# Optimization experiments

Hardware: AMD Instinct MI355X
Metric: run time of the kernel (lower is better)

The kernel has to match this reference:

```python
import jax, jax.numpy as jnp
import numpy as np

B, C, W = 32, 3, 512
KSIZE = 5
EPS = 8.0
ID_OFFSET = 4.0
SCALE = ID_OFFSET / (W - 1)            # identity_offset / (image_crop - 1)
DEF_OFF = (2.0 + SCALE) / 2.0          # deforming_offset
PIX_W = 2.0 / W                        # pixel width in [-1,1] coords

def _gauss_kernel2d(k):
    sigma = k * 0.15 + 0.35
    half = (k - 1) * 0.5
    x = np.linspace(-half, half, k)
    pdf = np.exp(-0.5 * (x / sigma) ** 2)
    k1 = pdf / pdf.sum()
    return np.outer(k1, k1).astype(np.float32)

def _samp_iden():
    seq = np.arange(-(W - 1), W, 2) / (W - 1.0)   # length W, identity coords
    gx = np.tile(seq, (W, 1))
    gy = gx.T
    return jnp.asarray(np.stack([gx, gy])[None].astype(np.float32))  # [1,2,W,W]

IDEN = _samp_iden()
GKER = jnp.broadcast_to(jnp.asarray(_gauss_kernel2d(KSIZE))[None, None], (2, 1, KSIZE, KSIZE))

def _blur(g):
    p = KSIZE // 2
    g = jnp.pad(g, ((0, 0), (0, 0), (p, p), (p, p)), mode='reflect')
    # depthwise conv over the 2 grid channels (groups=2)
    return jax.lax.conv_general_dilated(g, GKER, (1, 1), 'VALID', feature_group_count=2)

def _forward_grid(prim_grid):
    pg = _blur(prim_grid)
    sg = pg + IDEN                                   # prim -> samp
    # samp -> accu: conv_transpose with [1,-1] == first difference (leading zero)
    s = sg + DEF_OFF
    sx, sy = s[:, :1], s[:, 1:2]
    ax = sx - jnp.concatenate([jnp.zeros_like(sx[..., :1]), sx[..., :-1]], axis=3)
    ay = sy - jnp.concatenate([jnp.zeros_like(sy[:, :, :1]), sy[:, :, :-1]], axis=2)
    ag = jnp.concatenate([ax, ay], axis=1) / SCALE
    ag = jax.nn.relu(ag)                             # accu_clip
    # accu -> samp: conv_transpose with all-ones filter == cumulative sum
    a = ag * SCALE
    sx2 = jnp.cumsum(a[:, :1], axis=3)
    sy2 = jnp.cumsum(a[:, 1:2], axis=2)
    sg = jnp.concatenate([sx2, sy2], axis=1) - DEF_OFF
    pg = jnp.clip(sg - IDEN, -PIX_W * EPS, PIX_W * EPS)  # prim_clip
    return jnp.clip(pg + IDEN, -1.0, 1.0)                # samp_clip (hardtanh)

def _grid_sample(img, grid):
    # img [B,C,W,W], grid [B,W,W,2] in [-1,1]; bilinear, zeros padding, align_corners=True
    x = (grid[..., 0] + 1.0) * 0.5 * (W - 1)
    y = (grid[..., 1] + 1.0) * 0.5 * (W - 1)
    x0 = jnp.floor(x); y0 = jnp.floor(y)
    x1 = x0 + 1.0;     y1 = y0 + 1.0
    wx1 = x - x0; wx0 = 1.0 - wx1
    wy1 = y - y0; wy0 = 1.0 - wy1
    def gather(xi, yi):
        valid = ((xi >= 0) & (xi < W) & (yi >= 0) & (yi < W)).astype(img.dtype)
        xc = jnp.clip(xi, 0, W - 1).astype(jnp.int32)
        yc = jnp.clip(yi, 0, W - 1).astype(jnp.int32)
        v = jax.vmap(lambda im, yy, xx: im[:, yy, xx])(img, yc, xc)  # [B,C,W,W]
        return v * valid[:, None]
    return (gather(x0, y0) * (wx0 * wy0)[:, None] + gather(x1, y0) * (wx1 * wy0)[:, None]
          + gather(x0, y1) * (wx0 * wy1)[:, None] + gather(x1, y1) * (wx1 * wy1)[:, None])

def setup_inputs() -> dict:
    key = jax.random.key(0)
    k1, k2 = jax.random.split(key)
    image = jax.random.normal(k1, (B, C, W, W), dtype=jnp.float32)
    prim_grid = jax.random.normal(k2, (B, 2, W, W), dtype=jnp.float32) * 0.01
    return {"image": image, "prim_grid": prim_grid}

def reference(image, prim_grid):
    samp_grid = _forward_grid(prim_grid)
    binding_grid = jnp.transpose(samp_grid, (0, 2, 3, 1))  # [B,W,W,2]
    return _grid_sample(image, binding_grid)
```

## Files before the change

kernel.cpp:

```cpp
#include <hip/hip_runtime.h>
#include <math.h>

#define WID 512
#define NB  32
#define NC  3
#define WW  (WID * WID)

constexpr float SCALE_F   = (float)(4.0 / 511.0);
constexpr float DEF_OFF_F = (float)((2.0 + 4.0 / 511.0) * 0.5);
constexpr float CLIP_F    = 0.03125f;

__device__ __forceinline__ int refl(int r) {
  r = r < 0 ? -r : r;
  return r > WID - 1 ? 2 * (WID - 1) - r : r;
}

__device__ __forceinline__ float seqf(int i) {
  return ((float)(2 * i - 511)) / 511.0f;
}

__global__ __launch_bounds__(512)
void kx_kernel(const float* __restrict__ pg, float* __restrict__ gridx,
               float kw0, float kw1, float kw2) {
  const int lane = threadIdx.x & 63;
  const int wv   = threadIdx.x >> 6;
  const int R = blockIdx.x * 8 + wv;
  const int b = R >> 9;
  const int i = R & (WID - 1);
  const float* base = pg + (size_t)b * 2 * WW;

  float v[8] = {0.f,0.f,0.f,0.f,0.f,0.f,0.f,0.f};
  const int rows[5] = {refl(i - 2), refl(i - 1), i, refl(i + 1), refl(i + 2)};
  const float wts[5] = {kw0, kw1, kw2, kw1, kw0};
#pragma unroll
  for (int r = 0; r < 5; ++r) {
    const float4* p = (const float4*)(base + (size_t)rows[r] * WID + lane * 8);
    float4 A = p[0], Bq = p[1];
    float w = wts[r];
    v[0] += w * A.x;  v[1] += w * A.y;  v[2] += w * A.z;  v[3] += w * A.w;
    v[4] += w * Bq.x; v[5] += w * Bq.y; v[6] += w * Bq.z; v[7] += w * Bq.w;
  }

  float em1 = __shfl_up(v[7], 1, 64);
  float em2 = __shfl_up(v[6], 1, 64);
  float ep8 = __shfl_down(v[0], 1, 64);
  float ep9 = __shfl_down(v[1], 1, 64);
  if (lane == 0)  { em1 = v[1]; em2 = v[2]; }
  if (lane == 63) { ep8 = v[6]; ep9 = v[5]; }

  float h[8];
  h[0] = kw2 * v[0] + kw1 * (em1 + v[1]) + kw0 * (em2 + v[2]);
  h[1] = kw2 * v[1] + kw1 * (v[0] + v[2]) + kw0 * (em1 + v[3]);
#pragma unroll
  for (int k = 2; k < 6; ++k)
    h[k] = kw2 * v[k] + kw1 * (v[k - 1] + v[k + 1]) + kw0 * (v[k - 2] + v[k + 2]);
  h[6] = kw2 * v[6] + kw1 * (v[5] + v[7]) + kw0 * (v[4] + ep8);
  h[7] = kw2 * v[7] + kw1 * (v[6] + ep8) + kw0 * (v[5] + ep9);

  float s[8], a[8], p[8];
#pragma unroll
  for (int k = 0; k < 8; ++k) s[k] = h[k] + seqf(lane * 8 + k) + DEF_OFF_F;

  float sm1 = __shfl_up(s[7], 1, 64);
  if (lane == 0) sm1 = 0.0f;
  a[0] = fmaxf((s[0] - sm1) / SCALE_F, 0.0f) * SCALE_F;
#pragma unroll
  for (int k = 1; k < 8; ++k)
    a[k] = fmaxf((s[k] - s[k - 1]) / SCALE_F, 0.0f) * SCALE_F;

  p[0] = a[0];
#pragma unroll
  for (int k = 1; k < 8; ++k) p[k] = p[k - 1] + a[k];
  float incl = p[7];
#pragma unroll
  for (int off = 1; off < 64; off <<= 1) {
    float n = __shfl_up(incl, off, 64);
    if (lane >= off) incl += n;
  }
  float excl = incl - p[7];

  float og[8];
#pragma unroll
  for (int k = 0; k < 8; ++k) {
    float gx = seqf(lane * 8 + k);
    float d = (p[k] + excl) - DEF_OFF_F - gx;
    d = fminf(fmaxf(d, -CLIP_F), CLIP_F);
    og[k] = fminf(fmaxf(d + gx, -1.0f), 1.0f);
  }
  float4* o = (float4*)(gridx + ((size_t)b * WID + i) * WID + lane * 8);
  o[0] = make_float4(og[0], og[1], og[2], og[3]);
  o[1] = make_float4(og[4], og[5], og[6], og[7]);
}

#define KY1_ROWS 133
#define KY1_COLS 72

__global__ __launch_bounds__(256)
void ky1_kernel(const float* __restrict__ pg, float* __restrict__ gridy,
                float* __restrict__ qsum, float kw0, float kw1, float kw2) {
  const int q    = blockIdx.x & 3;
  const int tile = (blockIdx.x >> 2) & 7;
  const int b    = blockIdx.x >> 5;
  const int q0   = q << 7;
  const int gc0  = tile << 6;

  __shared__ float L[KY1_ROWS * KY1_COLS];
  __shared__ float ss[4][64];

  const float* src = pg + ((size_t)b * 2 + 1) * WW;
  for (int idx = threadIdx.x; idx < KY1_ROWS * 18; idx += 256) {
    int lr = idx / 18;
    int k  = idx - lr * 18;
    int gr = refl(q0 - 3 + lr);
    int gcb = gc0 - 4 + (k << 2);
    gcb = gcb < 0 ? 0 : (gcb > WID - 4 ? WID - 4 : gcb);
    float4 v = *(const float4*)(src + (size_t)gr * WID + gcb);
    *(float4*)(&L[lr * KY1_COLS + (k << 2)]) = v;
  }
  __syncthreads();

  const int j   = threadIdx.x & 63;
  const int seg = threadIdx.x >> 6;

  int jcc[5];
#pragma unroll
  for (int d = 0; d < 5; ++d)
    jcc[d] = refl(gc0 + j + d - 2) - gc0 + 4;

  auto HB = [&](int r) -> float {
    const float* Lr = &L[r * KY1_COLS];
    return kw2 * Lr[jcc[2]] + kw1 * (Lr[jcc[1]] + Lr[jcc[3]])
         + kw0 * (Lr[jcc[0]] + Lr[jcc[4]]);
  };

  const int lri0 = seg * 32 + 2;
  float hm2 = HB(lri0 - 2);
  float hm1 = HB(lri0 - 1);
  float hc  = HB(lri0);
  float hp1 = HB(lri0 + 1);
  float hp2 = HB(lri0 + 2);

  const int istart = q0 + seg * 32 - 1;
  float areg[32];
  float sprev = 0.0f, suma = 0.0f;
#pragma unroll
  for (int k = 0; k <= 32; ++k) {
    float blur = kw2 * hc + kw1 * (hm1 + hp1) + kw0 * (hm2 + hp2);
    float s = blur + seqf(istart + k) + DEF_OFF_F;
    if (k == 0) {
      sprev = (q == 0 && seg == 0) ? 0.0f : s;
    } else {
      float a = fmaxf((s - sprev) / SCALE_F, 0.0f) * SCALE_F;
      areg[k - 1] = a;
      suma += a;
      sprev = s;
    }
    if (k < 32) {
      hm2 = hm1; hm1 = hc; hc = hp1; hp1 = hp2;
      hp2 = HB(lri0 + k + 3);
    }
  }

  ss[seg][j] = suma;
  __syncthreads();
  float off = 0.0f;
#pragma unroll
  for (int w = 0; w < 3; ++w)
    if (w < seg) off += ss[w][j];
  if (seg == 3)
    qsum[((size_t)b * 4 + q) * WID + gc0 + j] = off + suma;

  float* ob = gridy + (size_t)b * WW + (size_t)(q0 + seg * 32) * WID + gc0 + j;
  float cum = off;
#pragma unroll
  for (int k = 0; k < 32; ++k) {
    cum += areg[k];
    ob[(size_t)k * WID] = cum;
  }
}

__global__ __launch_bounds__(128)
void ky2_kernel(float* __restrict__ gridy, const float* __restrict__ qsum) {
  const int b = blockIdx.x >> 9;
  const int i = blockIdx.x & 511;
  const int q = i >> 7;
  const int j4 = threadIdx.x << 2;
  const float* qs = qsum + (size_t)b * 4 * WID + j4;
  float ox = 0.f, oy = 0.f, oz = 0.f, ow = 0.f;
  for (int w = 0; w < q; ++w) {
    float4 t = *(const float4*)(qs + (size_t)w * WID);
    ox += t.x; oy += t.y; oz += t.z; ow += t.w;
  }
  const float gy = seqf(i);
  float* p = gridy + ((size_t)b * WID + i) * WID + j4;
  float4 v = *(float4*)p;
  auto fin = [&](float c) -> float {
    float d = c - DEF_OFF_F - gy;
    d = fminf(fmaxf(d, -CLIP_F), CLIP_F);
    return fminf(fmaxf(d + gy, -1.0f), 1.0f);
  };
  v.x = fin(v.x + ox); v.y = fin(v.y + oy);
  v.z = fin(v.z + oz); v.w = fin(v.w + ow);
  *(float4*)p = v;
}

#define STILE  8
#define SROWS  24
#define LSTR   516
#define SAMP_BLOCKS (NB * NC * (WID / STILE))

__global__ __launch_bounds__(512)
void sample_kernel(const float* __restrict__ img, const float* __restrict__ gridx,
                   const float* __restrict__ gridy, float* __restrict__ out) {
  const int nb = (blockIdx.x & 7) * (SAMP_BLOCKS / 8) + (blockIdx.x >> 3);
  const int rt = nb & 63;
  const int bc = nb >> 6;
  const int b  = bc / 3;
  const int c  = bc - b * 3;
  const int r0 = rt * STILE;

  __shared__ float tile[SROWS * LSTR];

  const float* ic = img + ((size_t)b * NC + c) * WW;
#pragma unroll
  for (int it = 0; it < (SROWS * 128) / 512; ++it) {
    int idx = it * 512 + threadIdx.x;
    int lr = idx >> 7;
    int c4 = (idx & 127) << 2;
    int gr = r0 - 8 + lr;
    gr = gr < 0 ? 0 : (gr > WID - 1 ? WID - 1 : gr);
    float4 vq = *(const float4*)(ic + (size_t)gr * WID + c4);
    *(float4*)(&tile[lr * LSTR + c4]) = vq;
  }
  __syncthreads();

  const int j = threadIdx.x;
  float* ob = out + ((size_t)b * NC + c) * WW;
#pragma unroll
  for (int r = 0; r < STILE; ++r) {
    const int i = r0 + r;
    const size_t gidx = ((size_t)b * WID + i) * WID + j;
    float gx = gridx[gidx];
    float gy = gridy[gidx];
    float x = (gx + 1.0f) * 0.5f * (float)(WID - 1);
    float y = (gy + 1.0f) * 0.5f * (float)(WID - 1);
    float x0f = floorf(x), y0f = floorf(y);
    int x0 = (int)x0f, y0 = (int)y0f;
    float wx1 = x - x0f, wx0 = 1.0f - wx1;
    float wy1 = y - y0f, wy0 = 1.0f - wy1;
    int x1 = x0 + 1, y1 = y0 + 1;
    int x1c = x1 > WID - 1 ? WID - 1 : x1;
    int y1c = y1 > WID - 1 ? WID - 1 : y1;
    float vx1 = x1 < WID ? 1.0f : 0.0f;
    float vy1 = y1 < WID ? 1.0f : 0.0f;

    float w00 = wx0 * wy0;
    float w01 = wx1 * wy0 * vx1;
    float w10 = wx0 * wy1 * vy1;
    float w11 = wx1 * wy1 * vx1 * vy1;

    int ly0 = y0 - r0 + 8;
    int ly1 = y1c - r0 + 8;
    float v00 = tile[ly0 * LSTR + x0];
    float v01 = tile[ly0 * LSTR + x1c];
    float v10 = tile[ly1 * LSTR + x0];
    float v11 = tile[ly1 * LSTR + x1c];

    ob[(size_t)i * WID + j] = w00 * v00 + w01 * v01 + w10 * v10 + w11 * v11;
  }
}

extern "C" void kernel_launch(void* const* d_in, const int* in_sizes, int n_in,
                              void* d_out, int out_size, void* d_ws, size_t ws_size,
                              hipStream_t stream) {
  const float* img = (const float*)d_in[0];
  const float* pg  = (const float*)d_in[1];
  float* out = (float*)d_out;

  float* gridx = (float*)d_ws;
  float* gridy = gridx + (size_t)NB * WW;

  const size_t grids_bytes = (size_t)2 * NB * WW * sizeof(float);
  const size_t qsum_bytes  = (size_t)NB * 4 * WID * sizeof(float);
  float* qsum = (ws_size >= grids_bytes + qsum_bytes)
              ? (float*)((char*)d_ws + grids_bytes)
              : (float*)d_out;

  double sigma = 5.0 * 0.15 + 0.35;
  double p0 = exp(-0.5 * (2.0 / sigma) * (2.0 / sigma));
  double p1 = exp(-0.5 * (1.0 / sigma) * (1.0 / sigma));
  double p2 = 1.0;
  double sum = 2.0 * p0 + 2.0 * p1 + p2;
  float kw0 = (float)(p0 / sum), kw1 = (float)(p1 / sum), kw2 = (float)(p2 / sum);

  kx_kernel<<<NB * WID / 8, 512, 0, stream>>>(pg, gridx, kw0, kw1, kw2);
  ky1_kernel<<<NB * 8 * 4, 256, 0, stream>>>(pg, gridy, qsum, kw0, kw1, kw2);
  ky2_kernel<<<NB * WID, 128, 0, stream>>>(gridy, qsum);
  sample_kernel<<<SAMP_BLOCKS, 512, 0, stream>>>(img, gridx, gridy, out);
}
```

Before: 272.4 us.

## Merge grid kernels, fold y-fixup into sampler, use direct global-to-LDS loads

Combines the x-grid and y-grid scan kernels into one launch that branches on block index, with the y path now using 512 threads and 16-row segments. When the workspace is large enough, the separate y-offset pass is dropped: the sampler adds the quarter-sum offset and applies the clip itself, which saves a full read-modify-write of gridy. The sampler's image tile is now filled with global_load_lds and no longer uses a padded LDS stride. This cuts launches and memory traffic, at the cost of LDS bank conflicts from the unpadded stride and a larger shared allocation in the merged kernel.

```diff
diff --git a/kernel.cpp b/kernel.cpp
--- a/kernel.cpp
+++ b/kernel.cpp
@@ -19,163 +19,169 @@
   return ((float)(2 * i - 511)) / 511.0f;
 }
 
-__global__ __launch_bounds__(512)
-void kx_kernel(const float* __restrict__ pg, float* __restrict__ gridx,
-               float kw0, float kw1, float kw2) {
-  const int lane = threadIdx.x & 63;
-  const int wv   = threadIdx.x >> 6;
-  const int R = blockIdx.x * 8 + wv;
-  const int b = R >> 9;
-  const int i = R & (WID - 1);
-  const float* base = pg + (size_t)b * 2 * WW;
-
-  float v[8] = {0.f,0.f,0.f,0.f,0.f,0.f,0.f,0.f};
-  const int rows[5] = {refl(i - 2), refl(i - 1), i, refl(i + 1), refl(i + 2)};
-  const float wts[5] = {kw0, kw1, kw2, kw1, kw0};
-#pragma unroll
-  for (int r = 0; r < 5; ++r) {
-    const float4* p = (const float4*)(base + (size_t)rows[r] * WID + lane * 8);
-    float4 A = p[0], Bq = p[1];
-    float w = wts[r];
-    v[0] += w * A.x;  v[1] += w * A.y;  v[2] += w * A.z;  v[3] += w * A.w;
-    v[4] += w * Bq.x; v[5] += w * Bq.y; v[6] += w * Bq.z; v[7] += w * Bq.w;
-  }
-
-  float em1 = __shfl_up(v[7], 1, 64);
-  float em2 = __shfl_up(v[6], 1, 64);
-  float ep8 = __shfl_down(v[0], 1, 64);
-  float ep9 = __shfl_down(v[1], 1, 64);
-  if (lane == 0)  { em1 = v[1]; em2 = v[2]; }
-  if (lane == 63) { ep8 = v[6]; ep9 = v[5]; }
-
-  float h[8];
-  h[0] = kw2 * v[0] + kw1 * (em1 + v[1]) + kw0 * (em2 + v[2]);
-  h[1] = kw2 * v[1] + kw1 * (v[0] + v[2]) + kw0 * (em1 + v[3]);
-#pragma unroll
-  for (int k = 2; k < 6; ++k)
-    h[k] = kw2 * v[k] + kw1 * (v[k - 1] + v[k + 1]) + kw0 * (v[k - 2] + v[k + 2]);
-  h[6] = kw2 * v[6] + kw1 * (v[5] + v[7]) + kw0 * (v[4] + ep8);
-  h[7] = kw2 * v[7] + kw1 * (v[6] + ep8) + kw0 * (v[5] + ep9);
-
-  float s[8], a[8], p[8];
-#pragma unroll
-  for (int k = 0; k < 8; ++k) s[k] = h[k] + seqf(lane * 8 + k) + DEF_OFF_F;
-
-  float sm1 = __shfl_up(s[7], 1, 64);
-  if (lane == 0) sm1 = 0.0f;
-  a[0] = fmaxf((s[0] - sm1) / SCALE_F, 0.0f) * SCALE_F;
-#pragma unroll
-  for (int k = 1; k < 8; ++k)
-    a[k] = fmaxf((s[k] - s[k - 1]) / SCALE_F, 0.0f) * SCALE_F;
-
-  p[0] = a[0];
-#pragma unroll
-  for (int k = 1; k < 8; ++k) p[k] = p[k - 1] + a[k];
-  float incl = p[7];
-#pragma unroll
-  for (int off = 1; off < 64; off <<= 1) {
-    float n = __shfl_up(incl, off, 64);
-    if (lane >= off) incl += n;
-  }
-  float excl = incl - p[7];
-
-  float og[8];
-#pragma unroll
-  for (int k = 0; k < 8; ++k) {
-    float gx = seqf(lane * 8 + k);
-    float d = (p[k] + excl) - DEF_OFF_F - gx;
-    d = fminf(fmaxf(d, -CLIP_F), CLIP_F);
-    og[k] = fminf(fmaxf(d + gx, -1.0f), 1.0f);
-  }
-  float4* o = (float4*)(gridx + ((size_t)b * WID + i) * WID + lane * 8);
-  o[0] = make_float4(og[0], og[1], og[2], og[3]);
-  o[1] = make_float4(og[4], og[5], og[6], og[7]);
+__device__ __forceinline__ void gl_lds16(const float* g, float* l) {
+  __builtin_amdgcn_global_load_lds(
+      (const __attribute__((address_space(1))) void*)g,
+      (__attribute__((address_space(3))) void*)l, 16, 0, 0);
 }
 
 #define KY1_ROWS 133
 #define KY1_COLS 72
 
-__global__ __launch_bounds__(256)
-void ky1_kernel(const float* __restrict__ pg, float* __restrict__ gridy,
-                float* __restrict__ qsum, float kw0, float kw1, float kw2) {
-  const int q    = blockIdx.x & 3;
-  const int tile = (blockIdx.x >> 2) & 7;
-  const int b    = blockIdx.x >> 5;
-  const int q0   = q << 7;
-  const int gc0  = tile << 6;
-
-  __shared__ float L[KY1_ROWS * KY1_COLS];
-  __shared__ float ss[4][64];
-
-  const float* src = pg + ((size_t)b * 2 + 1) * WW;
-  for (int idx = threadIdx.x; idx < KY1_ROWS * 18; idx += 256) {
-    int lr = idx / 18;
-    int k  = idx - lr * 18;
-    int gr = refl(q0 - 3 + lr);
-    int gcb = gc0 - 4 + (k << 2);
-    gcb = gcb < 0 ? 0 : (gcb > WID - 4 ? WID - 4 : gcb);
-    float4 v = *(const float4*)(src + (size_t)gr * WID + gcb);
-    *(float4*)(&L[lr * KY1_COLS + (k << 2)]) = v;
-  }
-  __syncthreads();
-
-  const int j   = threadIdx.x & 63;
-  const int seg = threadIdx.x >> 6;
-
-  int jcc[5];
-#pragma unroll
-  for (int d = 0; d < 5; ++d)
-    jcc[d] = refl(gc0 + j + d - 2) - gc0 + 4;
-
-  auto HB = [&](int r) -> float {
-    const float* Lr = &L[r * KY1_COLS];
-    return kw2 * Lr[jcc[2]] + kw1 * (Lr[jcc[1]] + Lr[jcc[3]])
-         + kw0 * (Lr[jcc[0]] + Lr[jcc[4]]);
-  };
-
-  const int lri0 = seg * 32 + 2;
-  float hm2 = HB(lri0 - 2);
-  float hm1 = HB(lri0 - 1);
-  float hc  = HB(lri0);
-  float hp1 = HB(lri0 + 1);
-  float hp2 = HB(lri0 + 2);
-
-  const int istart = q0 + seg * 32 - 1;
-  float areg[32];
-  float sprev = 0.0f, suma = 0.0f;
-#pragma unroll
-  for (int k = 0; k <= 32; ++k) {
-    float blur = kw2 * hc + kw1 * (hm1 + hp1) + kw0 * (hm2 + hp2);
-    float s = blur + seqf(istart + k) + DEF_OFF_F;
-    if (k == 0) {
-      sprev = (q == 0 && seg == 0) ? 0.0f : s;
-    } else {
-      float a = fmaxf((s - sprev) / SCALE_F, 0.0f) * SCALE_F;
-      areg[k - 1] = a;
-      suma += a;
-      sprev = s;
-    }
-    if (k < 32) {
-      hm2 = hm1; hm1 = hc; hc = hp1; hp1 = hp2;
-      hp2 = HB(lri0 + k + 3);
-    }
-  }
-
-  ss[seg][j] = suma;
-  __syncthreads();
-  float off = 0.0f;
-#pragma unroll
-  for (int w = 0; w < 3; ++w)
-    if (w < seg) off += ss[w][j];
-  if (seg == 3)
-    qsum[((size_t)b * 4 + q) * WID + gc0 + j] = off + suma;
-
-  float* ob = gridy + (size_t)b * WW + (size_t)(q0 + seg * 32) * WID + gc0 + j;
-  float cum = off;
-#pragma unroll
-  for (int k = 0; k < 32; ++k) {
-    cum += areg[k];
-    ob[(size_t)k * WID] = cum;
+__global__ __launch_bounds__(512)
+void grid_kernel(const float* __restrict__ pg, float* __restrict__ gridx,
+                 float* __restrict__ gridy, float* __restrict__ qsum,
+                 float kw0, float kw1, float kw2) {
+  if (blockIdx.x < 2048) {
+    const int lane = threadIdx.x & 63;
+    const int wv   = threadIdx.x >> 6;
+    const int R = blockIdx.x * 8 + wv;
+    const int b = R >> 9;
+    const int i = R & (WID - 1);
+    const float* base = pg + (size_t)b * 2 * WW;
+
+    float v[8] = {0.f,0.f,0.f,0.f,0.f,0.f,0.f,0.f};
+    const int rows[5] = {refl(i - 2), refl(i - 1), i, refl(i + 1), refl(i + 2)};
+    const float wts[5] = {kw0, kw1, kw2, kw1, kw0};
+#pragma unroll
+    for (int r = 0; r < 5; ++r) {
+      const float4* p = (const float4*)(base + (size_t)rows[r] * WID + lane * 8);
+      float4 A = p[0], Bq = p[1];
+      float w = wts[r];
+      v[0] += w * A.x;  v[1] += w * A.y;  v[2] += w * A.z;  v[3] += w * A.w;
+      v[4] += w * Bq.x; v[5] += w * Bq.y; v[6] += w * Bq.z; v[7] += w * Bq.w;
+    }
+
+    float em1 = __shfl_up(v[7], 1, 64);
+    float em2 = __shfl_up(v[6], 1, 64);
+    float ep8 = __shfl_down(v[0], 1, 64);
+    float ep9 = __shfl_down(v[1], 1, 64);
+    if (lane == 0)  { em1 = v[1]; em2 = v[2]; }
+    if (lane == 63) { ep8 = v[6]; ep9 = v[5]; }
+
+    float h[8];
+    h[0] = kw2 * v[0] + kw1 * (em1 + v[1]) + kw0 * (em2 + v[2]);
+    h[1] = kw2 * v[1] + kw1 * (v[0] + v[2]) + kw0 * (em1 + v[3]);
+#pragma unroll
+    for (int k = 2; k < 6; ++k)
+      h[k] = kw2 * v[k] + kw1 * (v[k - 1] + v[k + 1]) + kw0 * (v[k - 2] + v[k + 2]);
+    h[6] = kw2 * v[6] + kw1 * (v[5] + v[7]) + kw0 * (v[4] + ep8);
+    h[7] = kw2 * v[7] + kw1 * (v[6] + ep8) + kw0 * (v[5] + ep9);
+
+    float s[8], a[8], p[8];
+#pragma unroll
+    for (int k = 0; k < 8; ++k) s[k] = h[k] + seqf(lane * 8 + k) + DEF_OFF_F;
+
+    float sm1 = __shfl_up(s[7], 1, 64);
+    if (lane == 0) sm1 = 0.0f;
+    a[0] = fmaxf((s[0] - sm1) / SCALE_F, 0.0f) * SCALE_F;
+#pragma unroll
+    for (int k = 1; k < 8; ++k)
+      a[k] = fmaxf((s[k] - s[k - 1]) / SCALE_F, 0.0f) * SCALE_F;
+
+    p[0] = a[0];
+#pragma unroll
+    for (int k = 1; k < 8; ++k) p[k] = p[k - 1] + a[k];
+    float incl = p[7];
+#pragma unroll
+    for (int off = 1; off < 64; off <<= 1) {
+      float n = __shfl_up(incl, off, 64);
+      if (lane >= off) incl += n;
+    }
+    float excl = incl - p[7];
+
+    float og[8];
+#pragma unroll
+    for (int k = 0; k < 8; ++k) {
+      float gx = seqf(lane * 8 + k);
+      float d = (p[k] + excl) - DEF_OFF_F - gx;
+      d = fminf(fmaxf(d, -CLIP_F), CLIP_F);
+      og[k] = fminf(fmaxf(d + gx, -1.0f), 1.0f);
+    }
+    float4* o = (float4*)(gridx + ((size_t)b * WID + i) * WID + lane * 8);
+    o[0] = make_float4(og[0], og[1], og[2], og[3]);
+    o[1] = make_float4(og[4], og[5], og[6], og[7]);
+  } else {
+    const int bid  = blockIdx.x - 2048;
+    const int q    = bid & 3;
+    const int tile = (bid >> 2) & 7;
+    const int b    = bid >> 5;
+    const int q0   = q << 7;
+    const int gc0  = tile << 6;
+
+    __shared__ float L[KY1_ROWS * KY1_COLS];
+    __shared__ float ss[8][64];
+
+    const float* src = pg + ((size_t)b * 2 + 1) * WW;
+    for (int idx = threadIdx.x; idx < KY1_ROWS * 18; idx += 512) {
+      int lr = idx / 18;
+      int k  = idx - lr * 18;
+      int gr = refl(q0 - 3 + lr);
+      int gcb = gc0 - 4 + (k << 2);
+      gcb = gcb < 0 ? 0 : (gcb > WID - 4 ? WID - 4 : gcb);
+      float4 v = *(const float4*)(src + (size_t)gr * WID + gcb);
+      *(float4*)(&L[lr * KY1_COLS + (k << 2)]) = v;
+    }
+    __syncthreads();
+
+    const int j   = threadIdx.x & 63;
+    const int seg = threadIdx.x >> 6;
+
+    int jcc[5];
+#pragma unroll
+    for (int d = 0; d < 5; ++d)
+      jcc[d] = refl(gc0 + j + d - 2) - gc0 + 4;
+
+    auto HB = [&](int r) -> float {
+      const float* Lr = &L[r * KY1_COLS];
+      return kw2 * Lr[jcc[2]] + kw1 * (Lr[jcc[1]] + Lr[jcc[3]])
+           + kw0 * (Lr[jcc[0]] + Lr[jcc[4]]);
+    };
+
+    const int lri0 = seg * 16 + 2;
+    float hm2 = HB(lri0 - 2);
+    float hm1 = HB(lri0 - 1);
+    float hc  = HB(lri0);
+    float hp1 = HB(lri0 + 1);
+    float hp2 = HB(lri0 + 2);
+
+    const int istart = q0 + seg * 16 - 1;
+    float areg[16];
+    float sprev = 0.0f, suma = 0.0f;
+#pragma unroll
+    for (int k = 0; k <= 16; ++k) {
+      float blur = kw2 * hc + kw1 * (hm1 + hp1) + kw0 * (hm2 + hp2);
+      float s = blur + seqf(istart + k) + DEF_OFF_F;
+      if (k == 0) {
+        sprev = (q == 0 && seg == 0) ? 0.0f : s;
+      } else {
+        float a = fmaxf((s - sprev) / SCALE_F, 0.0f) * SCALE_F;
+        areg[k - 1] = a;
+        suma += a;
+        sprev = s;
+      }
+      if (k < 16) {
+        hm2 = hm1; hm1 = hc; hc = hp1; hp1 = hp2;
+        hp2 = HB(lri0 + k + 3);
+      }
+    }
+
+    ss[seg][j] = suma;
+    __syncthreads();
+    float off = 0.0f;
+#pragma unroll
+    for (int w = 0; w < 7; ++w)
+      if (w < seg) off += ss[w][j];
+    if (seg == 7)
+      qsum[((size_t)b * 4 + q) * WID + gc0 + j] = off + suma;
+
+    float* ob = gridy + (size_t)b * WW + (size_t)(q0 + seg * 16) * WID + gc0 + j;
+    float cum = off;
+#pragma unroll
+    for (int k = 0; k < 16; ++k) {
+      cum += areg[k];
+      ob[(size_t)k * WID] = cum;
+    }
   }
 }
 
@@ -206,12 +212,13 @@
 
 #define STILE  8
 #define SROWS  24
-#define LSTR   516
 #define SAMP_BLOCKS (NB * NC * (WID / STILE))
 
+template<bool FUSEY>
 __global__ __launch_bounds__(512)
 void sample_kernel(const float* __restrict__ img, const float* __restrict__ gridx,
-                   const float* __restrict__ gridy, float* __restrict__ out) {
+                   const float* __restrict__ gridy, const float* __restrict__ qsum,
+                   float* __restrict__ out) {
   const int nb = (blockIdx.x & 7) * (SAMP_BLOCKS / 8) + (blockIdx.x >> 3);
   const int rt = nb & 63;
   const int bc = nb >> 6;
@@ -219,22 +226,29 @@
   const int c  = bc - b * 3;
   const int r0 = rt * STILE;
 
-  __shared__ float tile[SROWS * LSTR];
+  __shared__ float tile[SROWS * WID];
 
   const float* ic = img + ((size_t)b * NC + c) * WW;
 #pragma unroll
-  for (int it = 0; it < (SROWS * 128) / 512; ++it) {
-    int idx = it * 512 + threadIdx.x;
-    int lr = idx >> 7;
-    int c4 = (idx & 127) << 2;
+  for (int it = 0; it < 6; ++it) {
+    int chunk = it * 512 + threadIdx.x;
+    int lr = chunk >> 7;
+    int c4 = (chunk & 127) << 2;
     int gr = r0 - 8 + lr;
     gr = gr < 0 ? 0 : (gr > WID - 1 ? WID - 1 : gr);
-    float4 vq = *(const float4*)(ic + (size_t)gr * WID + c4);
-    *(float4*)(&tile[lr * LSTR + c4]) = vq;
+    gl_lds16(ic + (size_t)gr * WID + c4, &tile[lr * WID + c4]);
   }
   __syncthreads();
 
   const int j = threadIdx.x;
+
+  float offy = 0.0f;
+  if (FUSEY) {
+    const int q = r0 >> 7;
+    const float* qs = qsum + (size_t)b * 4 * WID + j;
+    for (int w = 0; w < q; ++w) offy += qs[(size_t)w * WID];
+  }
+
   float* ob = out + ((size_t)b * NC + c) * WW;
 #pragma unroll
   for (int r = 0; r < STILE; ++r) {
@@ -242,6 +256,12 @@
     const size_t gidx = ((size_t)b * WID + i) * WID + j;
     float gx = gridx[gidx];
     float gy = gridy[gidx];
+    if (FUSEY) {
+      const float gyl = seqf(i);
+      float d = (gy + offy) - DEF_OFF_F - gyl;
+      d = fminf(fmaxf(d, -CLIP_F), CLIP_F);
+      gy = fminf(fmaxf(d + gyl, -1.0f), 1.0f);
+    }
     float x = (gx + 1.0f) * 0.5f * (float)(WID - 1);
     float y = (gy + 1.0f) * 0.5f * (float)(WID - 1);
     float x0f = floorf(x), y0f = floorf(y);
@@ -261,10 +281,10 @@
 
     int ly0 = y0 - r0 + 8;
     int ly1 = y1c - r0 + 8;
-    float v00 = tile[ly0 * LSTR + x0];
-    float v01 = tile[ly0 * LSTR + x1c];
-    float v10 = tile[ly1 * LSTR + x0];
-    float v11 = tile[ly1 * LSTR + x1c];
+    float v00 = tile[ly0 * WID + x0];
+    float v01 = tile[ly0 * WID + x1c];
+    float v10 = tile[ly1 * WID + x0];
+    float v11 = tile[ly1 * WID + x1c];
 
     ob[(size_t)i * WID + j] = w00 * v00 + w01 * v01 + w10 * v10 + w11 * v11;
   }
@@ -282,9 +302,9 @@
 
   const size_t grids_bytes = (size_t)2 * NB * WW * sizeof(float);
   const size_t qsum_bytes  = (size_t)NB * 4 * WID * sizeof(float);
-  float* qsum = (ws_size >= grids_bytes + qsum_bytes)
-              ? (float*)((char*)d_ws + grids_bytes)
-              : (float*)d_out;
+  const bool ws_fits = (ws_size >= grids_bytes + qsum_bytes);
+  float* qsum = ws_fits ? (float*)((char*)d_ws + grids_bytes)
+                        : (float*)d_out;
 
   double sigma = 5.0 * 0.15 + 0.35;
   double p0 = exp(-0.5 * (2.0 / sigma) * (2.0 / sigma));
@@ -293,8 +313,14 @@
   double sum = 2.0 * p0 + 2.0 * p1 + p2;
   float kw0 = (float)(p0 / sum), kw1 = (float)(p1 / sum), kw2 = (float)(p2 / sum);
 
-  kx_kernel<<<NB * WID / 8, 512, 0, stream>>>(pg, gridx, kw0, kw1, kw2);
-  ky1_kernel<<<NB * 8 * 4, 256, 0, stream>>>(pg, gridy, qsum, kw0, kw1, kw2);
-  ky2_kernel<<<NB * WID, 128, 0, stream>>>(gridy, qsum);
-  sample_kernel<<<SAMP_BLOCKS, 512, 0, stream>>>(img, gridx, gridy, out);
-}
+  grid_kernel<<<2048 + NB * 32, 512, 0, stream>>>(pg, gridx, gridy, qsum,
+                                                  kw0, kw1, kw2);
+  if (ws_fits) {
+    sample_kernel<true><<<SAMP_BLOCKS, 512, 0, stream>>>(img, gridx, gridy,
+                                                         qsum, out);
+  } else {
+    ky2_kernel<<<NB * WID, 128, 0, stream>>>(gridy, qsum);
+    sample_kernel<false><<<SAMP_BLOCKS, 512, 0, stream>>>(img, gridx, gridy,
+                                                          qsum, out);
+  }
+}
```

Result: faster. 264.2 us (-3.0%).
